# Performance work log

Hardware: AMD Instinct MI355X
Metric: run time of the kernel (lower is better)

The kernel has to match this reference:

```python
import jax, jax.numpy as jnp
import numpy as np

T = 2048
HID = 4096
NH = 32
DN = 128   # qk_nope_head_dim
DR = 64    # qk_rope_head_dim
DV = 128   # v_head_dim
QLR = 1536 # q_lora_rank
KVLR = 512 # kv_lora_rank
EPS = 1e-6
THETA = 10000.0


def rmsnorm(x, g):
    return x * jax.lax.rsqrt(jnp.mean(x * x, axis=-1, keepdims=True) + EPS) * g


def apply_rope(x, positions):
    # x: [T, H, DR], interleaved (non-neox) rotation
    d = x.shape[-1]
    inv_freq = 1.0 / (THETA ** (jnp.arange(0, d, 2, dtype=jnp.float32) / d))
    f = positions.astype(jnp.float32)[:, None] * inv_freq  # [T, DR/2]
    cos = jnp.cos(f)[:, None, :]
    sin = jnp.sin(f)[:, None, :]
    x1 = x[..., 0::2]
    x2 = x[..., 1::2]
    o1 = x1 * cos - x2 * sin
    o2 = x2 * cos + x1 * sin
    return jnp.stack([o1, o2], axis=-1).reshape(x.shape)


def setup_inputs() -> dict:
    key = jax.random.key(0)
    ks = jax.random.split(key, 8)
    s = lambda k, sh, fan: jax.random.normal(k, sh, jnp.float32) * (fan ** -0.5)
    return {
        "positions": jnp.arange(T, dtype=jnp.int64),
        "hidden_states": jax.random.normal(ks[0], (T, HID), jnp.float32),
        "w_qa": s(ks[1], (HID, QLR), HID),
        "w_kva": s(ks[2], (HID, KVLR + DR), HID),
        "g_qa": jnp.ones((QLR,), jnp.float32),
        "w_qb": s(ks[3], (QLR, NH * (DN + DR)), QLR),
        "g_kva": jnp.ones((KVLR,), jnp.float32),
        "w_kvb": s(ks[4], (KVLR, NH * (DN + DV)), KVLR),
        "w_o": s(ks[5], (NH * DV, HID), NH * DV),
    }


def reference(positions, hidden_states, w_qa, w_kva, g_qa, w_qb, g_kva, w_kvb, w_o):
    scale = (DN + DR) ** -0.5
    # fused a-projections (low-rank)
    q_c = rmsnorm(hidden_states @ w_qa, g_qa)            # [T, QLR]
    kv = hidden_states @ w_kva                            # [T, KVLR+DR]
    kv_c, k_pe = kv[:, :KVLR], kv[:, KVLR:]
    # q up-projection, split nope/rope
    q = (q_c @ w_qb).reshape(T, NH, DN + DR)
    q_nope, q_pe = q[..., :DN], q[..., DN:]
    q_pe = apply_rope(q_pe, positions)                    # [T, NH, DR]
    k_pe = apply_rope(k_pe[:, None, :], positions)        # [T, 1, DR]
    # kv up-projection from compressed cache
    kv_up = (rmsnorm(kv_c, g_kva) @ w_kvb).reshape(T, NH, DN + DV)
    k_nope, v = kv_up[..., :DN], kv_up[..., DN:]
    qf = jnp.concatenate([q_nope, q_pe], axis=-1)         # [T, NH, DN+DR]
    kf = jnp.concatenate([k_nope, jnp.broadcast_to(k_pe, (T, NH, DR))], axis=-1)
    scores = jnp.einsum("qhd,khd->hqk", qf, kf) * scale   # [NH, T, T]
    causal = jnp.tril(jnp.ones((T, T), dtype=bool))
    scores = jnp.where(causal[None], scores, jnp.finfo(scores.dtype).min)
    probs = jax.nn.softmax(scores, axis=-1)
    attn = jnp.einsum("hqk,khd->qhd", probs, v)           # [T, NH, DV]
    return attn.reshape(T, NH * DV) @ w_o                 # [T, HID]
```

## Files before the change

kernel.cpp:

```cpp
#include <hip/hip_runtime.h>
#include <math.h>

typedef __bf16 bf16;
typedef __bf16 bf16x8 __attribute__((ext_vector_type(8)));
typedef __bf16 bf16x4 __attribute__((ext_vector_type(4)));
typedef float  f32x4  __attribute__((ext_vector_type(4)));

#define AS1C(p) ((const __attribute__((address_space(1))) void*)(p))
#define AS3(p)  ((__attribute__((address_space(3))) void*)(p))

template<bool OUT_BF16>
__global__ __launch_bounds__(256) void gemm_bf16(const bf16* __restrict__ A,
                                                 const bf16* __restrict__ Bt,
                                                 void* __restrict__ Cv,
                                                 int M, int N, int K)
{
    __shared__ bf16 As[128 * 32];
    __shared__ bf16 Bs[128 * 32];
    const int tid = threadIdx.x;
    const int lane = tid & 63, wid = tid >> 6;
    const int lg = lane >> 4, ll = lane & 15;
    const int wr = wid >> 1, wc = wid & 1;
    const int bm = blockIdx.y * 128, bn = blockIdx.x * 128;

    f32x4 acc[4][4] = {};

    const int srow = wid * 16 + (lane >> 2);
    const int schk = (lane & 3) * 8;
    const bf16* Ag  = A  + (size_t)(bm + srow) * K + schk;
    const bf16* Ag2 = Ag + (size_t)64 * K;
    const bf16* Bg  = Bt + (size_t)(bn + srow) * K + schk;
    const bf16* Bg2 = Bg + (size_t)64 * K;
    bf16* Al = As + srow * 32 + schk;
    bf16* Bl = Bs + srow * 32 + schk;

    for (int k0 = 0; k0 < K; k0 += 32) {
        __syncthreads();
        __builtin_amdgcn_global_load_lds(AS1C(Ag  + k0), AS3(Al),            16, 0, 0);
        __builtin_amdgcn_global_load_lds(AS1C(Ag2 + k0), AS3(Al + 64 * 32), 16, 0, 0);
        __builtin_amdgcn_global_load_lds(AS1C(Bg  + k0), AS3(Bl),            16, 0, 0);
        __builtin_amdgcn_global_load_lds(AS1C(Bg2 + k0), AS3(Bl + 64 * 32), 16, 0, 0);
        __syncthreads();

        bf16x8 af[4], bfr[4];
#pragma unroll
        for (int mi = 0; mi < 4; ++mi)
            af[mi] = *(const bf16x8*)(As + (wr * 64 + mi * 16 + ll) * 32 + lg * 8);
#pragma unroll
        for (int ni = 0; ni < 4; ++ni)
            bfr[ni] = *(const bf16x8*)(Bs + (wc * 64 + ni * 16 + ll) * 32 + lg * 8);
#pragma unroll
        for (int mi = 0; mi < 4; ++mi)
#pragma unroll
            for (int ni = 0; ni < 4; ++ni)
                acc[mi][ni] = __builtin_amdgcn_mfma_f32_16x16x32_bf16(
                    af[mi], bfr[ni], acc[mi][ni], 0, 0, 0);
    }

#pragma unroll
    for (int mi = 0; mi < 4; ++mi)
#pragma unroll
        for (int ni = 0; ni < 4; ++ni)
#pragma unroll
            for (int j = 0; j < 4; ++j) {
                int row = bm + wr * 64 + mi * 16 + lg * 4 + j;
                int col = bn + wc * 64 + ni * 16 + ll;
                if (col < N) {
                    float v = acc[mi][ni][j];
                    if (OUT_BF16) ((bf16*)Cv)[(size_t)row * N + col] = (bf16)v;
                    else          ((float*)Cv)[(size_t)row * N + col] = v;
                }
            }
}

__global__ __launch_bounds__(256) void transpose_cast(const float* __restrict__ src,
                                                      bf16* __restrict__ dst,
                                                      int R, int C)
{
    __shared__ float t[32][33];
    const int bx = blockIdx.x * 32, by = blockIdx.y * 32;
    const int x = threadIdx.x & 31, y = threadIdx.x >> 5;
#pragma unroll
    for (int k = 0; k < 4; ++k) {
        int r = by + y + k * 8, c = bx + x;
        t[y + k * 8][x] = (c < C) ? src[(size_t)r * C + c] : 0.0f;
    }
    __syncthreads();
#pragma unroll
    for (int k = 0; k < 4; ++k) {
        int c = bx + y + k * 8, r = by + x;
        dst[(size_t)c * R + r] = (bf16)t[x][y + k * 8];
    }
}

__global__ __launch_bounds__(256) void cast_f32_bf16(const float* __restrict__ src,
                                                     bf16* __restrict__ dst, int n)
{
    int i = (blockIdx.x * 256 + threadIdx.x) * 4;
    if (i < n) {
        float4 v = *(const float4*)(src + i);
        bf16x4 o = { (bf16)v.x, (bf16)v.y, (bf16)v.z, (bf16)v.w };
        *(bf16x4*)(dst + i) = o;
    }
}

__global__ __launch_bounds__(256) void rmsnorm1536_bf16(const float* __restrict__ x,
                                                        const float* __restrict__ g,
                                                        bf16* __restrict__ o)
{
    int row = blockIdx.x, tid = threadIdx.x;
    const float* p = x + (size_t)row * 1536;
    float v[6]; float ssum = 0.f;
#pragma unroll
    for (int u = 0; u < 6; ++u) { v[u] = p[tid + 256 * u]; ssum += v[u] * v[u]; }
    __shared__ float red[256];
    red[tid] = ssum; __syncthreads();
    for (int s = 128; s > 0; s >>= 1) {
        if (tid < s) red[tid] += red[tid + s];
        __syncthreads();
    }
    float inv = rsqrtf(red[0] * (1.0f / 1536.0f) + 1e-6f);
#pragma unroll
    for (int u = 0; u < 6; ++u)
        o[(size_t)row * 1536 + tid + 256 * u] = (bf16)(v[u] * inv * g[tid + 256 * u]);
}

__global__ __launch_bounds__(256) void kvpost(const float* __restrict__ kvraw,
                                              const float* __restrict__ g,
                                              bf16* __restrict__ kv_cn,
                                              bf16* __restrict__ k_pe)
{
    int row = blockIdx.x, tid = threadIdx.x;
    const float* src = kvraw + (size_t)row * 576;
    float v0 = src[tid], v1 = src[tid + 256];
    float ssum = v0 * v0 + v1 * v1;
    __shared__ float red[256];
    red[tid] = ssum; __syncthreads();
    for (int s = 128; s > 0; s >>= 1) {
        if (tid < s) red[tid] += red[tid + s];
        __syncthreads();
    }
    float inv = rsqrtf(red[0] * (1.0f / 512.0f) + 1e-6f);
    kv_cn[(size_t)row * 512 + tid]       = (bf16)(v0 * inv * g[tid]);
    kv_cn[(size_t)row * 512 + tid + 256] = (bf16)(v1 * inv * g[tid + 256]);
    if (tid < 32) {
        float x1 = src[512 + 2 * tid], x2 = src[512 + 2 * tid + 1];
        float fr = powf(10000.0f, -(float)tid * (1.0f / 32.0f));
        float f = (float)row * fr;
        float c, s; sincosf(f, &s, &c);
        k_pe[(size_t)row * 64 + 2 * tid]     = (bf16)(x1 * c - x2 * s);
        k_pe[(size_t)row * 64 + 2 * tid + 1] = (bf16)(x2 * c + x1 * s);
    }
}

__global__ __launch_bounds__(256) void qrope_scale(bf16* __restrict__ q)
{
    const float sc = 0.07216878364870322f;
    int t = blockIdx.x, tid = threadIdx.x;
    bf16* row = q + (size_t)t * 6144;
#pragma unroll
    for (int u = 0; u < 16; ++u) {
        int idx = tid + 256 * u;
        int col = (idx >> 7) * 192 + (idx & 127);
        row[col] = (bf16)((float)row[col] * sc);
    }
#pragma unroll
    for (int u = 0; u < 4; ++u) {
        int pid = tid + 256 * u;
        int h = pid >> 5, i = pid & 31;
        int col = h * 192 + 128 + 2 * i;
        float x1 = (float)row[col], x2 = (float)row[col + 1];
        float fr = powf(10000.0f, -(float)i * (1.0f / 32.0f));
        float f = (float)t * fr;
        float c, s; sincosf(f, &s, &c);
        row[col]     = (bf16)((x1 * c - x2 * s) * sc);
        row[col + 1] = (bf16)((x2 * c + x1 * s) * sc);
    }
}

__global__ __launch_bounds__(256) void attn_mfma(const bf16* __restrict__ Q,
                                                 const bf16* __restrict__ KV,
                                                 const bf16* __restrict__ KPE,
                                                 bf16* __restrict__ O)
{
    __shared__ bf16 Ks[64][200];
    __shared__ bf16 Vt[128][72];
    __shared__ bf16 Ps[4][16][72];

    const int h = blockIdx.y, qt = blockIdx.x;
    const int q0 = qt * 64;
    const int tid = threadIdx.x;
    const int lane = tid & 63, wid = tid >> 6;
    const int lg = lane >> 4, ll = lane & 15;

    bf16x8 qf[6];
    {
        const bf16* qrow = Q + (size_t)(q0 + wid * 16 + ll) * 6144 + h * 192;
#pragma unroll
        for (int dk = 0; dk < 6; ++dk)
            qf[dk] = *(const bf16x8*)(qrow + dk * 32 + lg * 8);
    }

    f32x4 accO[8] = {};
    float m_r[4], l_r[4];
#pragma unroll
    for (int j = 0; j < 4; ++j) { m_r[j] = -INFINITY; l_r[j] = 0.f; }

    const int vsk  = tid & 63;
    const int vsq0 = tid >> 6;

    for (int kt = 0; kt <= qt; ++kt) {
        const int k0 = kt * 64;
        __syncthreads();
        {
            int r = wid * 16 + (lane >> 2);
            int rg = lane & 3;
#pragma unroll
            for (int cb = 0; cb < 6; ++cb) {
                int c = cb * 4 + rg;
                bf16x8 v;
                if (cb < 4)
                    v = *(const bf16x8*)(KV + (size_t)(k0 + r) * 8192 + h * 256 + c * 8);
                else
                    v = *(const bf16x8*)(KPE + (size_t)(k0 + r) * 64 + (c - 16) * 8);
                *(bf16x8*)&Ks[r][c * 8] = v;
            }
        }
#pragma unroll
        for (int i = 0; i < 8; ++i) {
            int v4 = (vsq0 + i * 4) * 4;
            bf16x4 v = *(const bf16x4*)(KV + (size_t)(k0 + vsk) * 8192 + h * 256 + 128 + v4);
#pragma unroll
            for (int jj = 0; jj < 4; ++jj)
                Vt[v4 + jj][vsk] = v[jj];
        }
        __syncthreads();

        f32x4 sacc[4] = {};
#pragma unroll
        for (int dk = 0; dk < 6; ++dk) {
#pragma unroll
            for (int ni = 0; ni < 4; ++ni) {
                bf16x8 kf = *(const bf16x8*)&Ks[ni * 16 + ll][dk * 32 + lg * 8];
                sacc[ni] = __builtin_amdgcn_mfma_f32_16x16x32_bf16(qf[dk], kf, sacc[ni], 0, 0, 0);
            }
        }

        float sv[4][4];
        const bool diag = (kt == qt);
#pragma unroll
        for (int ni = 0; ni < 4; ++ni)
#pragma unroll
            for (int j = 0; j < 4; ++j) {
                float s = sacc[ni][j];
                if (diag) {
                    int qg = wid * 16 + lg * 4 + j;
                    int kg = ni * 16 + ll;
                    if (kg > qg) s = -3.0e38f;
                }
                sv[ni][j] = s;
            }
#pragma unroll
        for (int j = 0; j < 4; ++j) {
            float pm = fmaxf(fmaxf(sv[0][j], sv[1][j]), fmaxf(sv[2][j], sv[3][j]));
#pragma unroll
            for (int msk = 1; msk <= 8; msk <<= 1)
                pm = fmaxf(pm, __shfl_xor(pm, msk));
            float mn = fmaxf(m_r[j], pm);
            float al = __expf(m_r[j] - mn);
            float ps = 0.f;
#pragma unroll
            for (int ni = 0; ni < 4; ++ni) {
                float p = __expf(sv[ni][j] - mn);
                sv[ni][j] = p; ps += p;
            }
#pragma unroll
            for (int msk = 1; msk <= 8; msk <<= 1)
                ps += __shfl_xor(ps, msk);
            l_r[j] = l_r[j] * al + ps;
            m_r[j] = mn;
#pragma unroll
            for (int vt = 0; vt < 8; ++vt) accO[vt][j] *= al;
#pragma unroll
            for (int ni = 0; ni < 4; ++ni)
                Ps[wid][lg * 4 + j][ni * 16 + ll] = (bf16)sv[ni][j];
        }

        bf16x8 pa[2];
#pragma unroll
        for (int kb = 0; kb < 2; ++kb)
            pa[kb] = *(const bf16x8*)&Ps[wid][ll][kb * 32 + lg * 8];
#pragma unroll
        for (int vt = 0; vt < 8; ++vt) {
#pragma unroll
            for (int kb = 0; kb < 2; ++kb) {
                bf16x8 vf = *(const bf16x8*)&Vt[vt * 16 + ll][kb * 32 + lg * 8];
                accO[vt] = __builtin_amdgcn_mfma_f32_16x16x32_bf16(pa[kb], vf, accO[vt], 0, 0, 0);
            }
        }
    }

    float inv[4];
#pragma unroll
    for (int j = 0; j < 4; ++j) inv[j] = 1.0f / l_r[j];
#pragma unroll
    for (int vt = 0; vt < 8; ++vt)
#pragma unroll
        for (int j = 0; j < 4; ++j) {
            int row = q0 + wid * 16 + lg * 4 + j;
            O[(size_t)row * 4096 + h * 128 + vt * 16 + ll] = (bf16)(accO[vt][j] * inv[j]);
        }
}

extern "C" void kernel_launch(void* const* d_in, const int* in_sizes, int n_in,
                              void* d_out, int out_size, void* d_ws, size_t ws_size,
                              hipStream_t stream)
{
    (void)in_sizes; (void)n_in; (void)out_size; (void)ws_size;
    const float* hs    = (const float*)d_in[1];
    const float* w_qa  = (const float*)d_in[2];
    const float* w_kva = (const float*)d_in[3];
    const float* g_qa  = (const float*)d_in[4];
    const float* w_qb  = (const float*)d_in[5];
    const float* g_kva = (const float*)d_in[6];
    const float* w_kvb = (const float*)d_in[7];
    const float* w_o   = (const float*)d_in[8];
    float* out = (float*)d_out;

    char* w = (char*)d_ws;
    bf16* hsb   = (bf16*)w;                     w += (size_t)2048 * 4096 * 2;
    bf16* wqaT  = (bf16*)w;                     w += (size_t)1536 * 4096 * 2;
    bf16* wkvaT = (bf16*)w;                     w += (size_t)640  * 4096 * 2;
    bf16* wqbT  = (bf16*)w;                     w += (size_t)6144 * 1536 * 2;
    bf16* wkvbT = (bf16*)w;                     w += (size_t)8192 * 512  * 2;
    bf16* woT   = (bf16*)w;                     w += (size_t)4096 * 4096 * 2;
    float* q_c  = (float*)w;                    w += (size_t)2048 * 1536 * 4;
    float* kvraw= (float*)w;                    w += (size_t)2048 * 576  * 4;
    bf16* q_cn  = (bf16*)w;                     w += (size_t)2048 * 1536 * 2;
    bf16* kv_cn = (bf16*)w;                     w += (size_t)2048 * 512  * 2;
    bf16* k_pe  = (bf16*)w;                     w += (size_t)2048 * 64   * 2;
    bf16* kvup  = (bf16*)w;                     w += (size_t)2048 * 8192 * 2;
    bf16* qfin  = hsb;
    bf16* attnb = (bf16*)q_c;

    dim3 blk(256);
    cast_f32_bf16<<<8192, blk, 0, stream>>>(hs, hsb, 2048 * 4096);
    transpose_cast<<<dim3(48, 128),  blk, 0, stream>>>(w_qa,  wqaT,  4096, 1536);
    transpose_cast<<<dim3(20, 128),  blk, 0, stream>>>(w_kva, wkvaT, 4096, 576);
    transpose_cast<<<dim3(192, 48),  blk, 0, stream>>>(w_qb,  wqbT,  1536, 6144);
    transpose_cast<<<dim3(256, 16),  blk, 0, stream>>>(w_kvb, wkvbT, 512,  8192);
    transpose_cast<<<dim3(128, 128), blk, 0, stream>>>(w_o,   woT,   4096, 4096);

    gemm_bf16<false><<<dim3(12, 16), blk, 0, stream>>>(hsb, wqaT,  q_c,   2048, 1536, 4096);
    gemm_bf16<false><<<dim3(5,  16), blk, 0, stream>>>(hsb, wkvaT, kvraw, 2048, 576,  4096);

    rmsnorm1536_bf16<<<2048, blk, 0, stream>>>(q_c, g_qa, q_cn);
    kvpost<<<2048, blk, 0, stream>>>(kvraw, g_kva, kv_cn, k_pe);

    gemm_bf16<true><<<dim3(48, 16), blk, 0, stream>>>(q_cn, wqbT, qfin, 2048, 6144, 1536);
    qrope_scale<<<2048, blk, 0, stream>>>(qfin);

    gemm_bf16<true><<<dim3(64, 16), blk, 0, stream>>>(kv_cn, wkvbT, kvup, 2048, 8192, 512);

    attn_mfma<<<dim3(32, 32), blk, 0, stream>>>(qfin, kvup, k_pe, attnb);

    gemm_bf16<false><<<dim3(32, 16), blk, 0, stream>>>(attnb, woT, out, 2048, 4096, 4096);
}
```

Before: 997.9 us.

## Emit transposed V from kv-up GEMM and restructure attention with 128-row tiles and prefetch

The kv up-projection GEMM now writes the V half of each head as a transposed [head*128+d][token] buffer, so attention no longer transposes V with scalar LDS stores. The attention kernel moves to 512-thread blocks covering 128 query rows. It schedules the heaviest causal tiles first, prefetches the next K/V tile into registers while computing the current one, and uses XOR-swizzled LDS layouts to avoid bank conflicts. Waves whose rows lie fully above the current key tile skip the compute. The transposed V reuses the wqbT workspace, which is only safe because that weight is consumed before this point. The larger blocks raise register pressure.

Result: faster. 817.2 us (-18.1%).

```diff
diff --git a/kernel.cpp b/kernel.cpp
--- a/kernel.cpp
+++ b/kernel.cpp
@@ -9,10 +9,11 @@
 #define AS1C(p) ((const __attribute__((address_space(1))) void*)(p))
 #define AS3(p)  ((__attribute__((address_space(3))) void*)(p))
 
-template<bool OUT_BF16>
+template<int MODE>
 __global__ __launch_bounds__(256) void gemm_bf16(const bf16* __restrict__ A,
                                                  const bf16* __restrict__ Bt,
                                                  void* __restrict__ Cv,
+                                                 bf16* __restrict__ VT,
                                                  int M, int N, int K)
 {
     __shared__ bf16 As[128 * 32];
@@ -57,6 +58,8 @@
                     af[mi], bfr[ni], acc[mi][ni], 0, 0, 0);
     }
 
+    const bool vsplit = (MODE == 2) && (blockIdx.x & 1);
+    const int hh = bn >> 8;
 #pragma unroll
     for (int mi = 0; mi < 4; ++mi)
 #pragma unroll
@@ -64,11 +67,15 @@
 #pragma unroll
             for (int j = 0; j < 4; ++j) {
                 int row = bm + wr * 64 + mi * 16 + lg * 4 + j;
-                int col = bn + wc * 64 + ni * 16 + ll;
-                if (col < N) {
-                    float v = acc[mi][ni][j];
-                    if (OUT_BF16) ((bf16*)Cv)[(size_t)row * N + col] = (bf16)v;
-                    else          ((float*)Cv)[(size_t)row * N + col] = v;
+                int cl  = wc * 64 + ni * 16 + ll;
+                int col = bn + cl;
+                float v = acc[mi][ni][j];
+                if (MODE == 2) {
+                    if (vsplit) VT[(size_t)(hh * 128 + cl) * 2048 + row] = (bf16)v;
+                    else        ((bf16*)Cv)[(size_t)row * N + col] = (bf16)v;
+                } else if (col < N) {
+                    if (MODE == 1) ((bf16*)Cv)[(size_t)row * N + col] = (bf16)v;
+                    else           ((float*)Cv)[(size_t)row * N + col] = v;
                 }
             }
 }
@@ -178,84 +185,121 @@
     }
 }
 
-__global__ __launch_bounds__(256) void attn_mfma(const bf16* __restrict__ Q,
+__global__ __launch_bounds__(512) void attn_mfma(const bf16* __restrict__ Q,
                                                  const bf16* __restrict__ KV,
                                                  const bf16* __restrict__ KPE,
+                                                 const bf16* __restrict__ VT,
                                                  bf16* __restrict__ O)
 {
-    __shared__ bf16 Ks[64][200];
-    __shared__ bf16 Vt[128][72];
-    __shared__ bf16 Ps[4][16][72];
-
-    const int h = blockIdx.y, qt = blockIdx.x;
-    const int q0 = qt * 64;
+    __shared__ bf16 knS[64 * 128];
+    __shared__ bf16 kpS[64 * 64];
+    __shared__ bf16 vtS[128 * 64];
+    __shared__ bf16 psS[8 * 16 * 88];
+
+    const int h = blockIdx.y;
+    const int qtb = 15 - blockIdx.x;
+    const int q0 = qtb * 128;
     const int tid = threadIdx.x;
     const int lane = tid & 63, wid = tid >> 6;
     const int lg = lane >> 4, ll = lane & 15;
+    const int nt = 2 * qtb + 2;
+    const int qwave = q0 + wid * 16;
 
     bf16x8 qf[6];
     {
-        const bf16* qrow = Q + (size_t)(q0 + wid * 16 + ll) * 6144 + h * 192;
+        const bf16* qrow = Q + (size_t)(qwave + ll) * 6144 + h * 192;
 #pragma unroll
         for (int dk = 0; dk < 6; ++dk)
             qf[dk] = *(const bf16x8*)(qrow + dk * 32 + lg * 8);
     }
 
+    int knRow[2], knDst[2]; size_t knSrc[2];
+    int kpDst; size_t kpSrc;
+    int vtDst[2]; size_t vtSrc[2];
+#pragma unroll
+    for (int p = 0; p < 2; ++p) {
+        int f = tid + p * 512;
+        int r = f >> 4, c = f & 15;
+        knRow[p] = r;
+        knDst[p] = r * 128 + ((c ^ (r & 7)) * 8);
+        knSrc[p] = (size_t)r * 8192 + h * 256 + c * 8;
+    }
+    {
+        int r = tid >> 3, c = tid & 7;
+        kpDst = r * 64 + ((c ^ (r & 7)) * 8);
+        kpSrc = (size_t)r * 64 + c * 8;
+    }
+#pragma unroll
+    for (int p = 0; p < 2; ++p) {
+        int f = tid + p * 512;
+        int r = f >> 3, c = f & 7;
+        vtDst[p] = r * 64 + ((c ^ (r & 7)) * 8);
+        vtSrc[p] = (size_t)(h * 128 + r) * 2048 + c * 8;
+    }
+
+    bf16x8 rkn[2], rkp, rvt[2];
+#pragma unroll
+    for (int p = 0; p < 2; ++p) rkn[p] = *(const bf16x8*)(KV + knSrc[p]);
+    rkp = *(const bf16x8*)(KPE + kpSrc);
+#pragma unroll
+    for (int p = 0; p < 2; ++p) rvt[p] = *(const bf16x8*)(VT + vtSrc[p]);
+
     f32x4 accO[8] = {};
     float m_r[4], l_r[4];
 #pragma unroll
     for (int j = 0; j < 4; ++j) { m_r[j] = -INFINITY; l_r[j] = 0.f; }
 
-    const int vsk  = tid & 63;
-    const int vsq0 = tid >> 6;
-
-    for (int kt = 0; kt <= qt; ++kt) {
+    const int e7 = ll & 7;
+    bf16* psW = psS + wid * 16 * 88;
+
+    for (int kt = 0; kt < nt; ++kt) {
         const int k0 = kt * 64;
         __syncthreads();
-        {
-            int r = wid * 16 + (lane >> 2);
-            int rg = lane & 3;
-#pragma unroll
-            for (int cb = 0; cb < 6; ++cb) {
-                int c = cb * 4 + rg;
-                bf16x8 v;
-                if (cb < 4)
-                    v = *(const bf16x8*)(KV + (size_t)(k0 + r) * 8192 + h * 256 + c * 8);
-                else
-                    v = *(const bf16x8*)(KPE + (size_t)(k0 + r) * 64 + (c - 16) * 8);
-                *(bf16x8*)&Ks[r][c * 8] = v;
-            }
+#pragma unroll
+        for (int p = 0; p < 2; ++p) *(bf16x8*)(knS + knDst[p]) = rkn[p];
+        *(bf16x8*)(kpS + kpDst) = rkp;
+#pragma unroll
+        for (int p = 0; p < 2; ++p) *(bf16x8*)(vtS + vtDst[p]) = rvt[p];
+        __syncthreads();
+        if (kt + 1 < nt) {
+            const size_t kvo = (size_t)(k0 + 64) * 8192;
+            const size_t kpo = (size_t)(k0 + 64) * 64;
+#pragma unroll
+            for (int p = 0; p < 2; ++p) rkn[p] = *(const bf16x8*)(KV + kvo + knSrc[p]);
+            rkp = *(const bf16x8*)(KPE + kpo + kpSrc);
+#pragma unroll
+            for (int p = 0; p < 2; ++p) rvt[p] = *(const bf16x8*)(VT + (k0 + 64) + vtSrc[p]);
         }
-#pragma unroll
-        for (int i = 0; i < 8; ++i) {
-            int v4 = (vsq0 + i * 4) * 4;
-            bf16x4 v = *(const bf16x4*)(KV + (size_t)(k0 + vsk) * 8192 + h * 256 + 128 + v4);
-#pragma unroll
-            for (int jj = 0; jj < 4; ++jj)
-                Vt[v4 + jj][vsk] = v[jj];
-        }
-        __syncthreads();
+        if (k0 > qwave + 15) continue;
 
         f32x4 sacc[4] = {};
 #pragma unroll
-        for (int dk = 0; dk < 6; ++dk) {
+        for (int dk = 0; dk < 4; ++dk)
 #pragma unroll
             for (int ni = 0; ni < 4; ++ni) {
-                bf16x8 kf = *(const bf16x8*)&Ks[ni * 16 + ll][dk * 32 + lg * 8];
+                bf16x8 kf = *(const bf16x8*)(knS + (ni * 16 + ll) * 128 +
+                                             (((dk * 4 + lg) ^ e7) * 8));
                 sacc[ni] = __builtin_amdgcn_mfma_f32_16x16x32_bf16(qf[dk], kf, sacc[ni], 0, 0, 0);
             }
-        }
+#pragma unroll
+        for (int dk = 4; dk < 6; ++dk)
+#pragma unroll
+            for (int ni = 0; ni < 4; ++ni) {
+                bf16x8 kf = *(const bf16x8*)(kpS + (ni * 16 + ll) * 64 +
+                                             ((((dk - 4) * 4 + lg) ^ e7) * 8));
+                sacc[ni] = __builtin_amdgcn_mfma_f32_16x16x32_bf16(qf[dk], kf, sacc[ni], 0, 0, 0);
+            }
 
         float sv[4][4];
-        const bool diag = (kt == qt);
+        const bool needm = (k0 + 63 > qwave);
 #pragma unroll
         for (int ni = 0; ni < 4; ++ni)
 #pragma unroll
             for (int j = 0; j < 4; ++j) {
                 float s = sacc[ni][j];
-                if (diag) {
-                    int qg = wid * 16 + lg * 4 + j;
-                    int kg = ni * 16 + ll;
+                if (needm) {
+                    int qg = qwave + lg * 4 + j;
+                    int kg = k0 + ni * 16 + ll;
                     if (kg > qg) s = -3.0e38f;
                 }
                 sv[ni][j] = s;
@@ -283,21 +327,21 @@
             for (int vt = 0; vt < 8; ++vt) accO[vt][j] *= al;
 #pragma unroll
             for (int ni = 0; ni < 4; ++ni)
-                Ps[wid][lg * 4 + j][ni * 16 + ll] = (bf16)sv[ni][j];
+                psW[(lg * 4 + j) * 88 + ni * 16 + ll] = (bf16)sv[ni][j];
         }
 
         bf16x8 pa[2];
 #pragma unroll
         for (int kb = 0; kb < 2; ++kb)
-            pa[kb] = *(const bf16x8*)&Ps[wid][ll][kb * 32 + lg * 8];
-#pragma unroll
-        for (int vt = 0; vt < 8; ++vt) {
+            pa[kb] = *(const bf16x8*)(psW + ll * 88 + kb * 32 + lg * 8);
+#pragma unroll
+        for (int vt = 0; vt < 8; ++vt)
 #pragma unroll
             for (int kb = 0; kb < 2; ++kb) {
-                bf16x8 vf = *(const bf16x8*)&Vt[vt * 16 + ll][kb * 32 + lg * 8];
+                bf16x8 vf = *(const bf16x8*)(vtS + (vt * 16 + ll) * 64 +
+                                             (((kb * 4 + lg) ^ e7) * 8));
                 accO[vt] = __builtin_amdgcn_mfma_f32_16x16x32_bf16(pa[kb], vf, accO[vt], 0, 0, 0);
             }
-        }
     }
 
     float inv[4];
@@ -307,7 +351,7 @@
     for (int vt = 0; vt < 8; ++vt)
 #pragma unroll
         for (int j = 0; j < 4; ++j) {
-            int row = q0 + wid * 16 + lg * 4 + j;
+            int row = qwave + lg * 4 + j;
             O[(size_t)row * 4096 + h * 128 + vt * 16 + ll] = (bf16)(accO[vt][j] * inv[j]);
         }
 }
@@ -342,6 +386,7 @@
     bf16* kvup  = (bf16*)w;                     w += (size_t)2048 * 8192 * 2;
     bf16* qfin  = hsb;
     bf16* attnb = (bf16*)q_c;
+    bf16* Vtg   = wqbT;
 
     dim3 blk(256);
     cast_f32_bf16<<<8192, blk, 0, stream>>>(hs, hsb, 2048 * 4096);
@@ -351,18 +396,18 @@
     transpose_cast<<<dim3(256, 16),  blk, 0, stream>>>(w_kvb, wkvbT, 512,  8192);
     transpose_cast<<<dim3(128, 128), blk, 0, stream>>>(w_o,   woT,   4096, 4096);
 
-    gemm_bf16<false><<<dim3(12, 16), blk, 0, stream>>>(hsb, wqaT,  q_c,   2048, 1536, 4096);
-    gemm_bf16<false><<<dim3(5,  16), blk, 0, stream>>>(hsb, wkvaT, kvraw, 2048, 576,  4096);
+    gemm_bf16<0><<<dim3(12, 16), blk, 0, stream>>>(hsb, wqaT,  q_c,   nullptr, 2048, 1536, 4096);
+    gemm_bf16<0><<<dim3(5,  16), blk, 0, stream>>>(hsb, wkvaT, kvraw, nullptr, 2048, 576,  4096);
 
     rmsnorm1536_bf16<<<2048, blk, 0, stream>>>(q_c, g_qa, q_cn);
     kvpost<<<2048, blk, 0, stream>>>(kvraw, g_kva, kv_cn, k_pe);
 
-    gemm_bf16<true><<<dim3(48, 16), blk, 0, stream>>>(q_cn, wqbT, qfin, 2048, 6144, 1536);
+    gemm_bf16<1><<<dim3(48, 16), blk, 0, stream>>>(q_cn, wqbT, qfin, nullptr, 2048, 6144, 1536);
     qrope_scale<<<2048, blk, 0, stream>>>(qfin);
 
-    gemm_bf16<true><<<dim3(64, 16), blk, 0, stream>>>(kv_cn, wkvbT, kvup, 2048, 8192, 512);
-
-    attn_mfma<<<dim3(32, 32), blk, 0, stream>>>(qfin, kvup, k_pe, attnb);
-
-    gemm_bf16<false><<<dim3(32, 16), blk, 0, stream>>>(attnb, woT, out, 2048, 4096, 4096);
-}
+    gemm_bf16<2><<<dim3(64, 16), blk, 0, stream>>>(kv_cn, wkvbT, kvup, Vtg, 2048, 8192, 512);
+
+    attn_mfma<<<dim3(16, 32), dim3(512), 0, stream>>>(qfin, kvup, k_pe, Vtg, attnb);
+
+    gemm_bf16<0><<<dim3(32, 16), blk, 0, stream>>>(attnb, woT, out, nullptr, 2048, 4096, 4096);
+}
```
